# Performance work log

Measured on AMD Instinct MI355X. Metric: run time of the kernel, lower is better.

## Reference

```python
import jax, jax.numpy as jnp
import numpy as np

MAX_CACHE_LEN = 1024
B, S, D, H = 8, 512, 512, 8
DK = D // H


def setup_inputs() -> dict:
    key = jax.random.key(0)
    ks = jax.random.split(key, 11)
    w = lambda k: jax.random.normal(k, (D, D), jnp.float32) * 0.02
    b = lambda k: jax.random.normal(k, (D,), jnp.float32) * 0.02
    return {
        "x": jax.random.normal(ks[0], (B, S, D), jnp.float32),
        "prev_k": jax.random.normal(ks[1], (B, H, MAX_CACHE_LEN, DK), jnp.float32),
        "prev_v": jax.random.normal(ks[2], (B, H, MAX_CACHE_LEN, DK), jnp.float32),
        "Wq": w(ks[3]), "bq": b(ks[4]),
        "Wk": w(ks[5]), "bk": b(ks[6]),
        "Wv": w(ks[7]), "bv": b(ks[8]),
        "Wo": w(ks[9]), "bo": b(ks[10]),
        "offset": MAX_CACHE_LEN,  # cache already full (steady-state streaming)
    }


def reference(x, prev_k, prev_v, Wq, bq, Wk, bk, Wv, bv, Wo, bo, offset):
    Bx, Sx, Dx = x.shape
    Hx = prev_k.shape[1]
    dk = Dx // Hx
    # projections (torch Linear: y = x @ W.T + b), split into heads -> [B,H,S,dk]
    def proj(W, bias):
        return (x @ W.T + bias).reshape(Bx, Sx, Hx, dk).transpose(0, 2, 1, 3)
    q = proj(Wq, bq)
    k = jnp.concatenate([prev_k, proj(Wk, bk)], axis=2)
    v = jnp.concatenate([prev_v, proj(Wv, bv)], axis=2)
    # sliding-window narrow to last MAX_CACHE_LEN keys (static shapes under jit)
    k_full = k.shape[2]
    start = max(0, k_full - MAX_CACHE_LEN)
    k = k[:, :, start:, :]
    v = v[:, :, start:, :]
    k_len = k.shape[2]
    new_offset = min(offset + Sx, MAX_CACHE_LEN)
    # scores [B,H,S,k_len]
    scores = jnp.einsum("bhqd,bhkd->bhqk", q, k) * (dk ** -0.5)
    q_start = new_offset - Sx
    q_idx = jnp.arange(Sx)[:, None] + q_start
    k_idx = jnp.arange(k_len)[None, :]
    mask = q_idx < k_idx  # future keys masked
    scores = jnp.where(mask[None, None], -jnp.inf, scores)
    attn = jax.nn.softmax(scores, axis=-1)
    out = jnp.einsum("bhqk,bhkd->bhqd", attn, v)
    out = out.transpose(0, 2, 1, 3).reshape(Bx, Sx, Dx)
    out = out @ Wo.T + bo
    return out, k, v, jnp.asarray(new_offset, jnp.int64 if jax.config.x64_enabled else jnp.int32)
```

## Files before the change

### kernel.cpp

```cpp
#include <hip/hip_runtime.h>
#include <math.h>

#define B_  8
#define S_  512
#define D_  512
#define H_  8
#define DK_ 64
#define KL_ 1024

typedef __attribute__((ext_vector_type(8))) short bf16x8;
typedef __attribute__((ext_vector_type(4))) float f32x4;

__device__ __forceinline__ unsigned short f2bf(float f) {
    unsigned u = __float_as_uint(f);
    u += 0x7FFF + ((u >> 16) & 1);
    return (unsigned short)(u >> 16);
}
__device__ __forceinline__ void gld16(const void* g, void* l) {
    __builtin_amdgcn_global_load_lds(
        (const __attribute__((address_space(1))) unsigned int*)g,
        (__attribute__((address_space(3))) unsigned int*)l, 16, 0, 0);
}

__global__ __launch_bounds__(256)
void prep_kernel(const float* __restrict__ x,
                 const float* __restrict__ Wq, const float* __restrict__ Wk,
                 const float* __restrict__ Wv, const float* __restrict__ Wo,
                 const float* __restrict__ pk, const float* __restrict__ pv,
                 unsigned short* __restrict__ xb,
                 unsigned short* __restrict__ Wqb, unsigned short* __restrict__ Wkb,
                 unsigned short* __restrict__ Wvb, unsigned short* __restrict__ Wob,
                 float* __restrict__ kout, float* __restrict__ vout,
                 unsigned short* __restrict__ Kp, unsigned short* __restrict__ Vp,
                 float* __restrict__ off_out) {
    const int blk = blockIdx.x, t = threadIdx.x;
    if (blk == 0 && t == 0) off_out[0] = 1024.0f;

    if (blk < 1536) {
        const float* src; unsigned short* dst; int off;
        if (blk < 1024) {
            src = x; dst = xb; off = blk * 256 + t;
        } else {
            int widx = blk - 1024;
            int grp = widx >> 7, wb = widx & 127;
            const float* ws_[4]        = {Wq, Wk, Wv, Wo};
            unsigned short* wd_[4]     = {Wqb, Wkb, Wvb, Wob};
            src = ws_[grp]; dst = wd_[grp]; off = wb * 256 + t;
        }
        float4 v0 = ((const float4*)src)[off * 2];
        float4 v1 = ((const float4*)src)[off * 2 + 1];
        unsigned short tmp[8] = {f2bf(v0.x), f2bf(v0.y), f2bf(v0.z), f2bf(v0.w),
                                 f2bf(v1.x), f2bf(v1.y), f2bf(v1.z), f2bf(v1.w)};
        *(uint4*)&dst[off * 8] = *(uint4*)tmp;
        return;
    }

    __shared__ float Kl[64][68];
    __shared__ float Vl[64][68];
    const int pb = blk - 1536;
    const int kt = pb & 7, bh = pb >> 3;
    const float* Kg = pk + (bh * KL_ + 512 + kt * 64) * DK_;
    const float* Vg = pv + (bh * KL_ + 512 + kt * 64) * DK_;
    float* Ko = kout + (bh * KL_ + kt * 64) * DK_;
    float* Vo = vout + (bh * KL_ + kt * 64) * DK_;
    #pragma unroll
    for (int it = 0; it < 4; ++it) {
        int idx = t + it * 256;
        int row = idx >> 4, c4 = idx & 15;
        float4 kv = *(const float4*)&Kg[row * 64 + c4 * 4];
        float4 vv = *(const float4*)&Vg[row * 64 + c4 * 4];
        *(float4*)&Ko[row * 64 + c4 * 4] = kv;
        *(float4*)&Vo[row * 64 + c4 * 4] = vv;
        *(float4*)&Kl[row][c4 * 4] = kv;
        *(float4*)&Vl[row][c4 * 4] = vv;
    }
    __syncthreads();
    unsigned short* Kpb = Kp + (bh * 16 + kt) * 4096;
    unsigned short* Vpb = Vp + (bh * 16 + kt) * 4096;
    #pragma unroll
    for (int s = 0; s < 2; ++s) {
        int slot = t + s * 256;
        int c = slot >> 6, l = slot & 63;
        int nn = c >> 1, hf = c & 1;
        {
            int row = nn * 16 + (l & 15), col = hf * 32 + (l >> 4) * 8;
            unsigned short tmp[8];
            #pragma unroll
            for (int j = 0; j < 8; ++j) tmp[j] = f2bf(Kl[row][col + j]);
            *(uint4*)&Kpb[c * 512 + l * 8] = *(uint4*)tmp;
        }
        {
            int row0 = hf * 32 + (l >> 4) * 8, col = nn * 16 + (l & 15);
            unsigned short tmp[8];
            #pragma unroll
            for (int j = 0; j < 8; ++j) tmp[j] = f2bf(Vl[row0 + j][col]);
            *(uint4*)&Vpb[c * 512 + l * 8] = *(uint4*)tmp;
        }
    }
}

template<int MODE, int BM>
__device__ __forceinline__
void mfma_gemm_body(const unsigned short* __restrict__ A,
                    const unsigned short* __restrict__ Wb,
                    const float* __restrict__ bias,
                    float* __restrict__ C32, unsigned short* __restrict__ C16,
                    unsigned short* __restrict__ Pk) {
    constexpr int MM = BM / 32;
    __shared__ unsigned short As[BM * 32];
    __shared__ unsigned short Bs[64 * 32];
    const int t = threadIdx.x, l = t & 63, w = t >> 6;
    const int m16 = l & 15, quad = l >> 4;
    const int wm = w >> 1, wn = w & 1;
    const int bn = blockIdx.x, bm = blockIdx.y;
    const int lr = l >> 2, lc = (l & 3) * 8;

    f32x4 acc[MM][2] = {};
    const unsigned short* Ag = A + (bm * BM) * 512;
    const unsigned short* Wg = Wb + (bn * 64) * 512;

    for (int k0 = 0; k0 < 512; k0 += 32) {
        __syncthreads();
        #pragma unroll
        for (int q = 0; q < BM / 64; ++q) {
            int chunk = w * (BM / 64) + q;
            gld16(Ag + (chunk * 16 + lr) * 512 + k0 + lc, &As[chunk * 512 + l * 8]);
        }
        gld16(Wg + (w * 16 + lr) * 512 + k0 + lc, &Bs[w * 512 + l * 8]);
        __syncthreads();

        bf16x8 af[MM], bfr[2];
        #pragma unroll
        for (int mm = 0; mm < MM; ++mm)
            af[mm] = *(const bf16x8*)&As[(wm * (BM / 2) + mm * 16 + m16) * 32 + quad * 8];
        #pragma unroll
        for (int nn = 0; nn < 2; ++nn)
            bfr[nn] = *(const bf16x8*)&Bs[(wn * 32 + nn * 16 + m16) * 32 + quad * 8];
        #pragma unroll
        for (int mm = 0; mm < MM; ++mm)
            #pragma unroll
            for (int nn = 0; nn < 2; ++nn)
                acc[mm][nn] = __builtin_amdgcn_mfma_f32_16x16x32_bf16(
                    af[mm], bfr[nn], acc[mm][nn], 0, 0, 0);
    }

    if constexpr (MODE == 2 || MODE == 4) {
        __shared__ __attribute__((aligned(16))) unsigned short Ts[9216];
        #pragma unroll
        for (int mm = 0; mm < MM; ++mm)
            #pragma unroll
            for (int nn = 0; nn < 2; ++nn) {
                int n = bn * 64 + wn * 32 + nn * 16 + m16;
                float bv_ = bias[n];
                int d = n & 63;
                #pragma unroll
                for (int r = 0; r < 4; ++r) {
                    int ml = wm * (BM / 2) + mm * 16 + quad * 4 + r;
                    int m = bm * BM + ml;
                    float val = acc[mm][nn][r] + bv_;
                    int b = m >> 9, s = m & 511, h = n >> 6;
                    C32[((b * H_ + h) * KL_ + 512 + s) * DK_ + d] = val;
                    if (MODE == 2) Ts[ml * 72 + d]  = f2bf(val);
                    else           Ts[d * 136 + ml] = f2bf(val);
                }
            }
        __syncthreads();
        const int bh = (bm >> 2) * H_ + bn;
        const int kt0 = 8 + (bm & 3) * 2;
        #pragma unroll
        for (int T = 0; T < 2; ++T)
            #pragma unroll
            for (int cp = 0; cp < 2; ++cp) {
                int c = w * 2 + cp, nn = c >> 1, hf = c & 1;
                uint4 frag;
                if (MODE == 2)
                    frag = *(const uint4*)&Ts[(T * 64 + nn * 16 + (l & 15)) * 72
                                              + hf * 32 + (l >> 4) * 8];
                else
                    frag = *(const uint4*)&Ts[(nn * 16 + (l & 15)) * 136
                                              + T * 64 + hf * 32 + (l >> 4) * 8];
                *(uint4*)&Pk[((bh * 16 + kt0 + T) * 4096) + c * 512 + l * 8] = frag;
            }
    } else {
        #pragma unroll
        for (int mm = 0; mm < MM; ++mm)
            #pragma unroll
            for (int nn = 0; nn < 2; ++nn) {
                int n = bn * 64 + wn * 32 + nn * 16 + m16;
                float bv_ = bias[n];
                #pragma unroll
                for (int r = 0; r < 4; ++r) {
                    int m = bm * BM + wm * (BM / 2) + mm * 16 + quad * 4 + r;
                    float val = acc[mm][nn][r] + bv_;
                    if (MODE == 3) {
                        C32[m * 512 + n] = val;
                    } else {
                        int b = m >> 9, s = m & 511;
                        int h = n >> 6, d = n & 63;
                        C16[((b * H_ + h) * S_ + s) * DK_ + d] = f2bf(val * 0.125f);
                    }
                }
            }
    }
}

__global__ __launch_bounds__(256)
void qkv_mfma_kernel(const unsigned short* __restrict__ xb,
                     const unsigned short* __restrict__ Wqb, const float* __restrict__ bq,
                     const unsigned short* __restrict__ Wkb, const float* __restrict__ bk,
                     const unsigned short* __restrict__ Wvb, const float* __restrict__ bv,
                     unsigned short* __restrict__ Qb, float* __restrict__ kout,
                     float* __restrict__ vout,
                     unsigned short* __restrict__ Kp, unsigned short* __restrict__ Vp) {
    if (blockIdx.z == 0)      mfma_gemm_body<1, 128>(xb, Wqb, bq, nullptr, Qb, nullptr);
    else if (blockIdx.z == 1) mfma_gemm_body<2, 128>(xb, Wkb, bk, kout, nullptr, Kp);
    else                      mfma_gemm_body<4, 128>(xb, Wvb, bv, vout, nullptr, Vp);
}

__global__ __launch_bounds__(256)
void out_mfma_kernel(const unsigned short* __restrict__ Ob, const unsigned short* __restrict__ Wob,
                     const float* __restrict__ bo, float* __restrict__ C) {
    mfma_gemm_body<3, 64>(Ob, Wob, bo, C, nullptr, nullptr);
}

__global__ __launch_bounds__(128)
void attn_kernel(const unsigned short* __restrict__ Qb,
                 const unsigned short* __restrict__ Kp,
                 const unsigned short* __restrict__ Vp,
                 unsigned short* __restrict__ Ob) {
    const int bh = blockIdx.x, qg = blockIdx.y;
    const int t = threadIdx.x, l = t & 63, w = t >> 6;
    const int m16 = l & 15, quad = l >> 4;
    const int q0 = qg * 32;

    __shared__ __attribute__((aligned(16))) unsigned short Ps[2][32][72];
    __shared__ float comb[64][40];

    bf16x8 qf[2][2];
    #pragma unroll
    for (int qh = 0; qh < 2; ++qh)
        #pragma unroll
        for (int p = 0; p < 2; ++p)
            qf[qh][p] = *(const bf16x8*)(Qb + (bh * S_ + q0 + qh * 16 + m16) * DK_
                                            + p * 32 + quad * 8);

    f32x4 acc[2][4] = {};
    float psum[2][4] = {};

    const int ktmax = (543 + q0) >> 6;
    const unsigned short* Kpb = Kp + (bh * 16) * 4096;
    const unsigned short* Vpb = Vp + (bh * 16) * 4096;

    for (int kt = w; kt <= ktmax; kt += 2) {
        const unsigned short* kb = Kpb + kt * 4096;
        const unsigned short* vb = Vpb + kt * 4096;
        bf16x8 kf[4][2], vf[4][2];
        #pragma unroll
        for (int nn = 0; nn < 4; ++nn)
            #pragma unroll
            for (int hf = 0; hf < 2; ++hf) {
                kf[nn][hf] = *(const bf16x8*)(kb + ((nn * 2 + hf) * 64 + l) * 8);
                vf[nn][hf] = *(const bf16x8*)(vb + ((nn * 2 + hf) * 64 + l) * 8);
            }

        f32x4 sc[2][4];
        #pragma unroll
        for (int qh = 0; qh < 2; ++qh)
            #pragma unroll
            for (int nn = 0; nn < 4; ++nn) {
                sc[qh][nn][0] = sc[qh][nn][1] = sc[qh][nn][2] = sc[qh][nn][3] = 0.f;
                sc[qh][nn] = __builtin_amdgcn_mfma_f32_16x16x32_bf16(qf[qh][0], kf[nn][0], sc[qh][nn], 0, 0, 0);
                sc[qh][nn] = __builtin_amdgcn_mfma_f32_16x16x32_bf16(qf[qh][1], kf[nn][1], sc[qh][nn], 0, 0, 0);
            }

        if (kt == ktmax) {
            #pragma unroll
            for (int qh = 0; qh < 2; ++qh)
                #pragma unroll
                for (int nn = 0; nn < 4; ++nn) {
                    int key = kt * 64 + nn * 16 + m16;
                    #pragma unroll
                    for (int r = 0; r < 4; ++r)
                        if (key > 512 + q0 + qh * 16 + (quad << 2) + r)
                            sc[qh][nn][r] = -INFINITY;
                }
        }

        #pragma unroll
        for (int qh = 0; qh < 2; ++qh)
            #pragma unroll
            for (int nn = 0; nn < 4; ++nn)
                #pragma unroll
                for (int r = 0; r < 4; ++r) {
                    float p = __expf(sc[qh][nn][r]);
                    psum[qh][r] += p;
                    Ps[w][qh * 16 + (quad << 2) + r][nn * 16 + m16] = f2bf(p);
                }

        bf16x8 pf[2][2];
        #pragma unroll
        for (int qh = 0; qh < 2; ++qh)
            #pragma unroll
            for (int hf = 0; hf < 2; ++hf)
                pf[qh][hf] = *(const bf16x8*)&Ps[w][qh * 16 + m16][hf * 32 + quad * 8];
        #pragma unroll
        for (int qh = 0; qh < 2; ++qh)
            #pragma unroll
            for (int nn = 0; nn < 4; ++nn) {
                acc[qh][nn] = __builtin_amdgcn_mfma_f32_16x16x32_bf16(pf[qh][0], vf[nn][0], acc[qh][nn], 0, 0, 0);
                acc[qh][nn] = __builtin_amdgcn_mfma_f32_16x16x32_bf16(pf[qh][1], vf[nn][1], acc[qh][nn], 0, 0, 0);
            }
    }

    if (w == 0) {
        #pragma unroll
        for (int qh = 0; qh < 2; ++qh)
            #pragma unroll
            for (int nn = 0; nn < 4; ++nn)
                #pragma unroll
                for (int r = 0; r < 4; ++r)
                    comb[l][(qh * 4 + nn) * 4 + r] = acc[qh][nn][r];
        #pragma unroll
        for (int qh = 0; qh < 2; ++qh)
            #pragma unroll
            for (int r = 0; r < 4; ++r)
                comb[l][32 + qh * 4 + r] = psum[qh][r];
    }
    __syncthreads();
    if (w == 1) {
        #pragma unroll
        for (int qh = 0; qh < 2; ++qh)
            #pragma unroll
            for (int nn = 0; nn < 4; ++nn)
                #pragma unroll
                for (int r = 0; r < 4; ++r)
                    acc[qh][nn][r] += comb[l][(qh * 4 + nn) * 4 + r];
        float inv[2][4];
        #pragma unroll
        for (int qh = 0; qh < 2; ++qh)
            #pragma unroll
            for (int r = 0; r < 4; ++r) {
                float ps = psum[qh][r] + comb[l][32 + qh * 4 + r];
                ps += __shfl_xor(ps, 1);
                ps += __shfl_xor(ps, 2);
                ps += __shfl_xor(ps, 4);
                ps += __shfl_xor(ps, 8);
                inv[qh][r] = 1.f / ps;
            }
        unsigned short* Og = Ob + ((bh >> 3) * S_ + q0) * D_ + (bh & 7) * DK_;
        #pragma unroll
        for (int qh = 0; qh < 2; ++qh)
            #pragma unroll
            for (int r = 0; r < 4; ++r)
                #pragma unroll
                for (int nn = 0; nn < 4; ++nn)
                    Og[(qh * 16 + (quad << 2) + r) * D_ + nn * 16 + m16] =
                        f2bf(acc[qh][nn][r] * inv[qh][r]);
    }
}

extern "C" void kernel_launch(void* const* d_in, const int* in_sizes, int n_in,
                              void* d_out, int out_size, void* d_ws, size_t ws_size,
                              hipStream_t stream) {
    const float* x  = (const float*)d_in[0];
    const float* pk = (const float*)d_in[1];
    const float* pv = (const float*)d_in[2];
    const float* Wq = (const float*)d_in[3];
    const float* bq = (const float*)d_in[4];
    const float* Wk = (const float*)d_in[5];
    const float* bk = (const float*)d_in[6];
    const float* Wv = (const float*)d_in[7];
    const float* bv = (const float*)d_in[8];
    const float* Wo = (const float*)d_in[9];
    const float* bo = (const float*)d_in[10];

    float* out     = (float*)d_out;
    float* kout    = out + 2097152;
    float* vout    = kout + 4194304;
    float* off_out = vout + 4194304;

    unsigned short* xb  = (unsigned short*)d_ws;
    unsigned short* Wqb = xb + 2097152;
    unsigned short* Wkb = Wqb + 262144;
    unsigned short* Wvb = Wkb + 262144;
    unsigned short* Wob = Wvb + 262144;
    unsigned short* Qb  = Wob + 262144;
    unsigned short* Kp  = Qb + 2097152;
    unsigned short* Vp  = Kp + 4194304;
    unsigned short* Ob  = xb;

    prep_kernel<<<2048, 256, 0, stream>>>(x, Wq, Wk, Wv, Wo, pk, pv,
                                          xb, Wqb, Wkb, Wvb, Wob,
                                          kout, vout, Kp, Vp, off_out);
    qkv_mfma_kernel<<<dim3(8, 32, 3), 256, 0, stream>>>(xb, Wqb, bq, Wkb, bk, Wvb, bv,
                                                        Qb, kout, vout, Kp, Vp);
    attn_kernel<<<dim3(64, 16), 128, 0, stream>>>(Qb, Kp, Vp, Ob);
    out_mfma_kernel<<<dim3(8, 64), 256, 0, stream>>>(Ob, Wob, bo, out);
}
```

Baseline: 164.0 us.

## Move prev-cache copy into QKV kernel, use exp2 softmax, defer V loads

Moves the copy and bf16 repacking of the old K/V cache out of the prep kernel and into a fourth z-slice of the QKV GEMM launch, so it overlaps with projection work. Shared memory becomes one explicitly carved buffer so the GEMM and copy paths can share it, and launch bounds now request 4 blocks per CU. In attention, the Q scale folds in log2(e) so softmax can use exp2f, and the V fragment loads move after the QK MFMAs to reduce register pressure. The trade-off is a heavier QKV grid and possible LDS or occupancy limits from the larger shared buffer.

```diff
diff --git a/kernel.cpp b/kernel.cpp
--- a/kernel.cpp
+++ b/kernel.cpp
@@ -26,38 +26,38 @@
 void prep_kernel(const float* __restrict__ x,
                  const float* __restrict__ Wq, const float* __restrict__ Wk,
                  const float* __restrict__ Wv, const float* __restrict__ Wo,
-                 const float* __restrict__ pk, const float* __restrict__ pv,
                  unsigned short* __restrict__ xb,
                  unsigned short* __restrict__ Wqb, unsigned short* __restrict__ Wkb,
                  unsigned short* __restrict__ Wvb, unsigned short* __restrict__ Wob,
-                 float* __restrict__ kout, float* __restrict__ vout,
-                 unsigned short* __restrict__ Kp, unsigned short* __restrict__ Vp,
                  float* __restrict__ off_out) {
     const int blk = blockIdx.x, t = threadIdx.x;
     if (blk == 0 && t == 0) off_out[0] = 1024.0f;
 
-    if (blk < 1536) {
-        const float* src; unsigned short* dst; int off;
-        if (blk < 1024) {
-            src = x; dst = xb; off = blk * 256 + t;
-        } else {
-            int widx = blk - 1024;
-            int grp = widx >> 7, wb = widx & 127;
-            const float* ws_[4]        = {Wq, Wk, Wv, Wo};
-            unsigned short* wd_[4]     = {Wqb, Wkb, Wvb, Wob};
-            src = ws_[grp]; dst = wd_[grp]; off = wb * 256 + t;
-        }
-        float4 v0 = ((const float4*)src)[off * 2];
-        float4 v1 = ((const float4*)src)[off * 2 + 1];
-        unsigned short tmp[8] = {f2bf(v0.x), f2bf(v0.y), f2bf(v0.z), f2bf(v0.w),
-                                 f2bf(v1.x), f2bf(v1.y), f2bf(v1.z), f2bf(v1.w)};
-        *(uint4*)&dst[off * 8] = *(uint4*)tmp;
-        return;
-    }
-
-    __shared__ float Kl[64][68];
-    __shared__ float Vl[64][68];
-    const int pb = blk - 1536;
+    const float* src; unsigned short* dst; int off;
+    if (blk < 1024) {
+        src = x; dst = xb; off = blk * 256 + t;
+    } else {
+        int widx = blk - 1024;
+        int grp = widx >> 7, wb = widx & 127;
+        const float* ws_[4]        = {Wq, Wk, Wv, Wo};
+        unsigned short* wd_[4]     = {Wqb, Wkb, Wvb, Wob};
+        src = ws_[grp]; dst = wd_[grp]; off = wb * 256 + t;
+    }
+    float4 v0 = ((const float4*)src)[off * 2];
+    float4 v1 = ((const float4*)src)[off * 2 + 1];
+    unsigned short tmp[8] = {f2bf(v0.x), f2bf(v0.y), f2bf(v0.z), f2bf(v0.w),
+                             f2bf(v1.x), f2bf(v1.y), f2bf(v1.z), f2bf(v1.w)};
+    *(uint4*)&dst[off * 8] = *(uint4*)tmp;
+}
+
+__device__ __forceinline__
+void prev_copy_body(const float* __restrict__ pk, const float* __restrict__ pv,
+                    float* __restrict__ kout, float* __restrict__ vout,
+                    unsigned short* __restrict__ Kp, unsigned short* __restrict__ Vp,
+                    unsigned char* __restrict__ smem, int pb) {
+    float (*Kl)[68] = (float (*)[68])smem;
+    float (*Vl)[68] = (float (*)[68])(smem + 17408);
+    const int t = threadIdx.x;
     const int kt = pb & 7, bh = pb >> 3;
     const float* Kg = pk + (bh * KL_ + 512 + kt * 64) * DK_;
     const float* Vg = pv + (bh * KL_ + 512 + kt * 64) * DK_;
@@ -97,6 +97,7 @@
             *(uint4*)&Vpb[c * 512 + l * 8] = *(uint4*)tmp;
         }
     }
+    __syncthreads();
 }
 
 template<int MODE, int BM>
@@ -105,10 +106,11 @@
                     const unsigned short* __restrict__ Wb,
                     const float* __restrict__ bias,
                     float* __restrict__ C32, unsigned short* __restrict__ C16,
-                    unsigned short* __restrict__ Pk) {
+                    unsigned short* __restrict__ Pk,
+                    unsigned char* __restrict__ smem) {
     constexpr int MM = BM / 32;
-    __shared__ unsigned short As[BM * 32];
-    __shared__ unsigned short Bs[64 * 32];
+    unsigned short* As = (unsigned short*)smem;
+    unsigned short* Bs = (unsigned short*)(smem + BM * 64);
     const int t = threadIdx.x, l = t & 63, w = t >> 6;
     const int m16 = l & 15, quad = l >> 4;
     const int wm = w >> 1, wn = w & 1;
@@ -145,7 +147,7 @@
     }
 
     if constexpr (MODE == 2 || MODE == 4) {
-        __shared__ __attribute__((aligned(16))) unsigned short Ts[9216];
+        unsigned short* Ts = (unsigned short*)(smem + BM * 64 + 4096);
         #pragma unroll
         for (int mm = 0; mm < MM; ++mm)
             #pragma unroll
@@ -197,30 +199,39 @@
                     } else {
                         int b = m >> 9, s = m & 511;
                         int h = n >> 6, d = n & 63;
-                        C16[((b * H_ + h) * S_ + s) * DK_ + d] = f2bf(val * 0.125f);
+                        C16[((b * H_ + h) * S_ + s) * DK_ + d] =
+                            f2bf(val * 0.18033688011112042f);
                     }
                 }
             }
     }
 }
 
-__global__ __launch_bounds__(256)
+__global__ __launch_bounds__(256, 4)
 void qkv_mfma_kernel(const unsigned short* __restrict__ xb,
                      const unsigned short* __restrict__ Wqb, const float* __restrict__ bq,
                      const unsigned short* __restrict__ Wkb, const float* __restrict__ bk,
                      const unsigned short* __restrict__ Wvb, const float* __restrict__ bv,
                      unsigned short* __restrict__ Qb, float* __restrict__ kout,
                      float* __restrict__ vout,
-                     unsigned short* __restrict__ Kp, unsigned short* __restrict__ Vp) {
-    if (blockIdx.z == 0)      mfma_gemm_body<1, 128>(xb, Wqb, bq, nullptr, Qb, nullptr);
-    else if (blockIdx.z == 1) mfma_gemm_body<2, 128>(xb, Wkb, bk, kout, nullptr, Kp);
-    else                      mfma_gemm_body<4, 128>(xb, Wvb, bv, vout, nullptr, Vp);
-}
-
-__global__ __launch_bounds__(256)
+                     unsigned short* __restrict__ Kp, unsigned short* __restrict__ Vp,
+                     const float* __restrict__ pk, const float* __restrict__ pv) {
+    __shared__ __attribute__((aligned(16))) unsigned char smem[34816];
+    if (blockIdx.z == 0)      mfma_gemm_body<1, 128>(xb, Wqb, bq, nullptr, Qb, nullptr, smem);
+    else if (blockIdx.z == 1) mfma_gemm_body<2, 128>(xb, Wkb, bk, kout, nullptr, Kp, smem);
+    else if (blockIdx.z == 2) mfma_gemm_body<4, 128>(xb, Wvb, bv, vout, nullptr, Vp, smem);
+    else {
+        int pb0 = blockIdx.y * 8 + blockIdx.x;
+        prev_copy_body(pk, pv, kout, vout, Kp, Vp, smem, pb0);
+        prev_copy_body(pk, pv, kout, vout, Kp, Vp, smem, pb0 + 256);
+    }
+}
+
+__global__ __launch_bounds__(256, 4)
 void out_mfma_kernel(const unsigned short* __restrict__ Ob, const unsigned short* __restrict__ Wob,
                      const float* __restrict__ bo, float* __restrict__ C) {
-    mfma_gemm_body<3, 64>(Ob, Wob, bo, C, nullptr, nullptr);
+    __shared__ __attribute__((aligned(16))) unsigned char smem[8192];
+    mfma_gemm_body<3, 64>(Ob, Wob, bo, C, nullptr, nullptr, smem);
 }
 
 __global__ __launch_bounds__(128)
@@ -254,14 +265,12 @@
     for (int kt = w; kt <= ktmax; kt += 2) {
         const unsigned short* kb = Kpb + kt * 4096;
         const unsigned short* vb = Vpb + kt * 4096;
-        bf16x8 kf[4][2], vf[4][2];
+        bf16x8 kf[4][2];
         #pragma unroll
         for (int nn = 0; nn < 4; ++nn)
             #pragma unroll
-            for (int hf = 0; hf < 2; ++hf) {
+            for (int hf = 0; hf < 2; ++hf)
                 kf[nn][hf] = *(const bf16x8*)(kb + ((nn * 2 + hf) * 64 + l) * 8);
-                vf[nn][hf] = *(const bf16x8*)(vb + ((nn * 2 + hf) * 64 + l) * 8);
-            }
 
         f32x4 sc[2][4];
         #pragma unroll
@@ -272,6 +281,13 @@
                 sc[qh][nn] = __builtin_amdgcn_mfma_f32_16x16x32_bf16(qf[qh][0], kf[nn][0], sc[qh][nn], 0, 0, 0);
                 sc[qh][nn] = __builtin_amdgcn_mfma_f32_16x16x32_bf16(qf[qh][1], kf[nn][1], sc[qh][nn], 0, 0, 0);
             }
+
+        bf16x8 vf[4][2];
+        #pragma unroll
+        for (int nn = 0; nn < 4; ++nn)
+            #pragma unroll
+            for (int hf = 0; hf < 2; ++hf)
+                vf[nn][hf] = *(const bf16x8*)(vb + ((nn * 2 + hf) * 64 + l) * 8);
 
         if (kt == ktmax) {
             #pragma unroll
@@ -292,7 +308,7 @@
             for (int nn = 0; nn < 4; ++nn)
                 #pragma unroll
                 for (int r = 0; r < 4; ++r) {
-                    float p = __expf(sc[qh][nn][r]);
+                    float p = exp2f(sc[qh][nn][r]);
                     psum[qh][r] += p;
                     Ps[w][qh * 16 + (quad << 2) + r][nn * 16 + m16] = f2bf(p);
                 }
@@ -389,11 +405,10 @@
     unsigned short* Vp  = Kp + 4194304;
     unsigned short* Ob  = xb;
 
-    prep_kernel<<<2048, 256, 0, stream>>>(x, Wq, Wk, Wv, Wo, pk, pv,
-                                          xb, Wqb, Wkb, Wvb, Wob,
-                                          kout, vout, Kp, Vp, off_out);
-    qkv_mfma_kernel<<<dim3(8, 32, 3), 256, 0, stream>>>(xb, Wqb, bq, Wkb, bk, Wvb, bv,
-                                                        Qb, kout, vout, Kp, Vp);
+    prep_kernel<<<1536, 256, 0, stream>>>(x, Wq, Wk, Wv, Wo,
+                                          xb, Wqb, Wkb, Wvb, Wob, off_out);
+    qkv_mfma_kernel<<<dim3(8, 32, 4), 256, 0, stream>>>(xb, Wqb, bq, Wkb, bk, Wvb, bv,
+                                                        Qb, kout, vout, Kp, Vp, pk, pv);
     attn_kernel<<<dim3(64, 16), 128, 0, stream>>>(Qb, Kp, Vp, Ob);
     out_mfma_kernel<<<dim3(8, 64), 256, 0, stream>>>(Ob, Wob, bo, out);
 }
```

Measured after the change: 156.5 us. -4.5%, faster.
